# Optimization experiments

Hardware: AMD Instinct MI355X
Metric: run time of the kernel (lower is better)

The kernel has to match this reference:

```python
import jax, jax.numpy as jnp
import numpy as np

B = 4            # scenes
N = 100000       # points per scene
BN = B * N
M = 200000       # occupied target voxels
C_IMG = 64       # img_feat_dim
C_3D = 32        # INIT_DIM (3D feature width at p1 scale)
COORD_MAX = 256  # voxel grid extent per axis


def setup_inputs() -> dict:
    key = jax.random.key(0)
    k1, k2, k3, k4, k5, k6 = jax.random.split(key, 6)
    # batched voxel coords: col0 = batch idx, cols1:4 = xyz voxel coords
    bcol = jax.random.randint(k1, (M, 1), 0, B, dtype=jnp.int32)
    xyz = jax.random.randint(k2, (M, 3), 0, COORD_MAX, dtype=jnp.int32)
    tgt_coords = jnp.concatenate([bcol, xyz], axis=1)  # (M,4)
    # each point maps onto some target voxel (torch code asserts full validity)
    pts_idx = jax.random.randint(k3, (BN,), 0, M, dtype=jnp.int32)
    pfeat = jax.random.normal(k4, (BN, C_IMG), dtype=jnp.float32)
    tgt_feats = jax.random.normal(k5, (M, C_3D), dtype=jnp.float32)
    W_fuse = jax.random.normal(k6, (C_3D + C_IMG, C_3D), dtype=jnp.float32) * 0.05
    b_fuse = jnp.zeros((C_3D,), dtype=jnp.float32)
    return {"pfeat": pfeat, "tgt_feats": tgt_feats, "W_fuse": W_fuse,
            "b_fuse": b_fuse, "tgt_coords": tgt_coords, "pts_idx": pts_idx}


def reference(pfeat, tgt_feats, W_fuse, b_fuse, tgt_coords, pts_idx):
    # point voxel coords (stride-snapped in torch; identity here since points map to voxels)
    pts_coords = tgt_coords[pts_idx]                              # (BN,4)
    # --- key packing (mirrors _pack_keys with shift-to-nonnegative) ---
    xyz_all = jnp.concatenate([pts_coords[:, 1:], tgt_coords[:, 1:]], axis=0)
    shift = jnp.maximum(-xyz_all.min(axis=0), 0)
    pts_xyz = pts_coords[:, 1:] + shift
    tgt_xyz = tgt_coords[:, 1:] + shift
    max_xyz = jnp.maximum(pts_xyz.max(axis=0), tgt_xyz.max(axis=0))
    mx, my, mz = max_xyz[0] + 1, max_xyz[1] + 1, max_xyz[2] + 1

    def pack(b, xyz):
        return ((b * mx + xyz[:, 0]) * my + xyz[:, 1]) * mz + xyz[:, 2]

    pts_key = pack(pts_coords[:, 0], pts_xyz)                     # (BN,)
    tgt_key = pack(tgt_coords[:, 0], tgt_xyz)                     # (M,)
    # --- sort target keys, binary-search point keys (torch.sort + searchsorted) ---
    order = jnp.argsort(tgt_key)
    tgt_key_sorted = tgt_key[order]
    pos = jnp.minimum(jnp.searchsorted(tgt_key_sorted, pts_key), M - 1)
    tgt_idx = order[pos]                                          # (BN,) voxel each point lands in
    # --- scatter-mean of 2D point features into voxels (_scatter_mean) ---
    sums = jax.ops.segment_sum(pfeat, tgt_idx, num_segments=M)    # (M,C_IMG)
    cnt = jax.ops.segment_sum(jnp.ones((pfeat.shape[0], 1), pfeat.dtype),
                              tgt_idx, num_segments=M)            # (M,1)
    img_feat_u = sums / jnp.maximum(cnt, 1.0)
    # --- ME.cat + 1x1 MinkowskiConvolution fuse == concat + matmul ---
    fused = jnp.concatenate([tgt_feats, img_feat_u], axis=1)      # (M, C_3D+C_IMG)
    return fused @ W_fuse + b_fuse                                # (M, C_3D)
```

## Files before the change

kernel.cpp:

```cpp
#include <hip/hip_runtime.h>

#define HBITS 19
#define HSIZE (1u << HBITS)
#define HMASK (HSIZE - 1u)
#define EMPTY_KEY 0xFFFFFFFFu
#define SLOTS 8

__device__ __forceinline__ unsigned hash_key(unsigned k) {
    return (k * 2654435761u) >> (32 - HBITS);
}

__device__ __forceinline__ unsigned pack_key(int4 c) {
    return ((unsigned)c.x << 24) | ((unsigned)c.y << 16) |
           ((unsigned)c.z << 8) | (unsigned)c.w;
}

__global__ __launch_bounds__(256)
void build_hash(const int4* __restrict__ tgt_coords, int M,
                uint2* __restrict__ htab) {
    int v = blockIdx.x * blockDim.x + threadIdx.x;
    if (v >= M) return;
    unsigned key = pack_key(tgt_coords[v]);
    unsigned h = hash_key(key);
    while (true) {
        unsigned prev = atomicCAS(&htab[h].x, EMPTY_KEY, key);
        if (prev == EMPTY_KEY || prev == key) {
            atomicMin(&htab[h].y, (unsigned)v);
            break;
        }
        h = (h + 1u) & HMASK;
    }
}

__global__ __launch_bounds__(256)
void fill_slots(const int* __restrict__ pts_idx,
                const int4* __restrict__ tgt_coords,
                const uint2* __restrict__ htab,
                int BN,
                int* __restrict__ cnt,
                int* __restrict__ slotbuf,
                int* __restrict__ ohead,
                int* __restrict__ nxt) {
    int p = blockIdx.x * blockDim.x + threadIdx.x;
    if (p >= BN) return;
    int vox = pts_idx[p];
    unsigned key = pack_key(tgt_coords[vox]);
    unsigned h = hash_key(key);
    uint2 e = htab[h];
    while (e.x != key) { h = (h + 1u) & HMASK; e = htab[h]; }
    int c = (int)e.y;
    int idx = atomicAdd(&cnt[c], 1) + 1;
    if (idx < SLOTS) slotbuf[c * SLOTS + idx] = p;
    else             nxt[p] = atomicExch(&ohead[c], p);
}

#define VPB 8
__global__ __launch_bounds__(256)
void gather_mean(const float2* __restrict__ pf2,
                 const int* __restrict__ cnt,
                 const int4* __restrict__ slot4,
                 const int* __restrict__ ohead,
                 const int* __restrict__ nxt,
                 int M,
                 float2* __restrict__ mean2) {
    int t = threadIdx.x;
    int grp = t >> 5;
    int g   = t & 31;
    int v = blockIdx.x * VPB + grp;
    if (v >= M) return;

    int n = cnt[v] + 1;
    int4 sa = make_int4(0, 0, 0, 0), sb = make_int4(0, 0, 0, 0);
    if (n > 0) sa = slot4[(size_t)v * 2];
    if (n > 4) sb = slot4[(size_t)v * 2 + 1];
    float2 f0 = {0,0}, f1 = {0,0}, f2 = {0,0}, f3 = {0,0};
    float2 f4 = {0,0}, f5 = {0,0}, f6 = {0,0}, f7 = {0,0};
    if (n > 0) f0 = pf2[(size_t)sa.x * 32 + g];
    if (n > 1) f1 = pf2[(size_t)sa.y * 32 + g];
    if (n > 2) f2 = pf2[(size_t)sa.z * 32 + g];
    if (n > 3) f3 = pf2[(size_t)sa.w * 32 + g];
    if (n > 4) f4 = pf2[(size_t)sb.x * 32 + g];
    if (n > 5) f5 = pf2[(size_t)sb.y * 32 + g];
    if (n > 6) f6 = pf2[(size_t)sb.z * 32 + g];
    if (n > 7) f7 = pf2[(size_t)sb.w * 32 + g];
    float sx = ((f0.x + f1.x) + (f2.x + f3.x)) + ((f4.x + f5.x) + (f6.x + f7.x));
    float sy = ((f0.y + f1.y) + (f2.y + f3.y)) + ((f4.y + f5.y) + (f6.y + f7.y));
    if (n > SLOTS) {
        int p = ohead[v];
        while (p >= 0) {
            float2 f = pf2[(size_t)p * 32 + g];
            sx += f.x; sy += f.y;
            p = nxt[p];
        }
    }
    float inv = 1.0f / fmaxf((float)n, 1.0f);
    mean2[(size_t)v * 32 + g] = make_float2(sx * inv, sy * inv);
}

__global__ __launch_bounds__(256)
void matmul_scalar(const float4* __restrict__ tgt4,
                   const float4* __restrict__ mean4,
                   const float* __restrict__ W,
                   const float* __restrict__ bias,
                   int M,
                   float4* __restrict__ out4) {
    int v = blockIdx.x * blockDim.x + threadIdx.x;
    if (v >= M) return;

    float acc[32];
#pragma unroll
    for (int oc = 0; oc < 32; ++oc) acc[oc] = bias[oc];

    const float4* xr = tgt4 + (size_t)v * 8;
#pragma unroll 2
    for (int k4 = 0; k4 < 8; ++k4) {
        float4 x = xr[k4];
        const float* w0 = W + k4 * 4 * 32;
#pragma unroll
        for (int oc = 0; oc < 32; ++oc) {
            acc[oc] = fmaf(x.x, w0[oc],      acc[oc]);
            acc[oc] = fmaf(x.y, w0[32 + oc], acc[oc]);
            acc[oc] = fmaf(x.z, w0[64 + oc], acc[oc]);
            acc[oc] = fmaf(x.w, w0[96 + oc], acc[oc]);
        }
    }
    const float4* mr = mean4 + (size_t)v * 16;
#pragma unroll 2
    for (int k4 = 0; k4 < 16; ++k4) {
        float4 x = mr[k4];
        const float* w0 = W + (32 + k4 * 4) * 32;
#pragma unroll
        for (int oc = 0; oc < 32; ++oc) {
            acc[oc] = fmaf(x.x, w0[oc],      acc[oc]);
            acc[oc] = fmaf(x.y, w0[32 + oc], acc[oc]);
            acc[oc] = fmaf(x.z, w0[64 + oc], acc[oc]);
            acc[oc] = fmaf(x.w, w0[96 + oc], acc[oc]);
        }
    }

    float4* o = out4 + (size_t)v * 8;
#pragma unroll
    for (int q = 0; q < 8; ++q)
        o[q] = make_float4(acc[4 * q], acc[4 * q + 1], acc[4 * q + 2], acc[4 * q + 3]);
}

extern "C" void kernel_launch(void* const* d_in, const int* in_sizes, int n_in,
                              void* d_out, int out_size, void* d_ws, size_t ws_size,
                              hipStream_t stream) {
    const float* pfeat      = (const float*)d_in[0];
    const float* tgt_feats  = (const float*)d_in[1];
    const float* W_fuse     = (const float*)d_in[2];
    const float* b_fuse     = (const float*)d_in[3];
    const int*   tgt_coords = (const int*)d_in[4];
    const int*   pts_idx    = (const int*)d_in[5];
    float* out = (float*)d_out;

    const int M  = in_sizes[4] / 4;
    const int BN = in_sizes[5];

    char* ws = (char*)d_ws;
    uint2* htab    = (uint2*)ws;
    size_t off = (size_t)HSIZE * 8;
    int*   cnt     = (int*)(ws + off);              off += (size_t)M * 4;
    int*   ohead   = (int*)(ws + off);              off += (size_t)M * 4;
    int*   slotbuf = (int*)(ws + off);              off += (size_t)M * SLOTS * 4;
    int*   nxt     = (int*)(ws + off);              off += (size_t)BN * 4;
    float* mean    = (float*)(ws + off);

    size_t ff_bytes = (size_t)HSIZE * 8 + (size_t)M * 8;
    hipMemsetAsync(htab, 0xFF, ff_bytes, stream);

    const int TB = 256;
    build_hash<<<(M + TB - 1) / TB, TB, 0, stream>>>(
        (const int4*)tgt_coords, M, htab);
    fill_slots<<<(BN + TB - 1) / TB, TB, 0, stream>>>(
        pts_idx, (const int4*)tgt_coords, htab, BN, cnt, slotbuf, ohead, nxt);
    gather_mean<<<(M + VPB - 1) / VPB, TB, 0, stream>>>(
        (const float2*)pfeat, cnt, (const int4*)slotbuf, ohead, nxt, M,
        (float2*)mean);
    matmul_scalar<<<(M + TB - 1) / TB, TB, 0, stream>>>(
        (const float4*)tgt_feats, (const float4*)mean, W_fuse, b_fuse, M,
        (float4*)out);
}
```

Baseline: 282.6 us.

## Fuse scatter-mean gather with the 1x1 fuse matmul via shared memory

Merges the gather_mean and matmul_scalar kernels into one kernel. Each 32-lane group stages its voxel's 3D features and mean image features in shared memory, then each lane computes one output channel using a register-held column of W. This removes the round trip of the mean buffer through global memory and one kernel launch. In exchange every thread loads 96 weights per block and there is a block-wide barrier.

```diff
diff --git a/kernel.cpp b/kernel.cpp
--- a/kernel.cpp
+++ b/kernel.cpp
@@ -56,92 +56,73 @@
 
 #define VPB 8
 __global__ __launch_bounds__(256)
-void gather_mean(const float2* __restrict__ pf2,
+void gather_fuse(const float2* __restrict__ pf2,
+                 const float* __restrict__ tgtf,
                  const int* __restrict__ cnt,
                  const int4* __restrict__ slot4,
                  const int* __restrict__ ohead,
                  const int* __restrict__ nxt,
+                 const float* __restrict__ W,
+                 const float* __restrict__ bias,
                  int M,
-                 float2* __restrict__ mean2) {
+                 float* __restrict__ out) {
+    __shared__ __align__(16) float xs[VPB][104];
+
     int t = threadIdx.x;
     int grp = t >> 5;
     int g   = t & 31;
     int v = blockIdx.x * VPB + grp;
-    if (v >= M) return;
+    bool valid = (v < M);
 
-    int n = cnt[v] + 1;
-    int4 sa = make_int4(0, 0, 0, 0), sb = make_int4(0, 0, 0, 0);
-    if (n > 0) sa = slot4[(size_t)v * 2];
-    if (n > 4) sb = slot4[(size_t)v * 2 + 1];
-    float2 f0 = {0,0}, f1 = {0,0}, f2 = {0,0}, f3 = {0,0};
-    float2 f4 = {0,0}, f5 = {0,0}, f6 = {0,0}, f7 = {0,0};
-    if (n > 0) f0 = pf2[(size_t)sa.x * 32 + g];
-    if (n > 1) f1 = pf2[(size_t)sa.y * 32 + g];
-    if (n > 2) f2 = pf2[(size_t)sa.z * 32 + g];
-    if (n > 3) f3 = pf2[(size_t)sa.w * 32 + g];
-    if (n > 4) f4 = pf2[(size_t)sb.x * 32 + g];
-    if (n > 5) f5 = pf2[(size_t)sb.y * 32 + g];
-    if (n > 6) f6 = pf2[(size_t)sb.z * 32 + g];
-    if (n > 7) f7 = pf2[(size_t)sb.w * 32 + g];
-    float sx = ((f0.x + f1.x) + (f2.x + f3.x)) + ((f4.x + f5.x) + (f6.x + f7.x));
-    float sy = ((f0.y + f1.y) + (f2.y + f3.y)) + ((f4.y + f5.y) + (f6.y + f7.y));
-    if (n > SLOTS) {
-        int p = ohead[v];
-        while (p >= 0) {
-            float2 f = pf2[(size_t)p * 32 + g];
-            sx += f.x; sy += f.y;
-            p = nxt[p];
+    if (valid) {
+        int n = cnt[v] + 1;
+        int4 sa = make_int4(0, 0, 0, 0), sb = make_int4(0, 0, 0, 0);
+        if (n > 0) sa = slot4[(size_t)v * 2];
+        if (n > 4) sb = slot4[(size_t)v * 2 + 1];
+        float2 f0 = {0,0}, f1 = {0,0}, f2 = {0,0}, f3 = {0,0};
+        float2 f4 = {0,0}, f5 = {0,0}, f6 = {0,0}, f7 = {0,0};
+        if (n > 0) f0 = pf2[(size_t)sa.x * 32 + g];
+        if (n > 1) f1 = pf2[(size_t)sa.y * 32 + g];
+        if (n > 2) f2 = pf2[(size_t)sa.z * 32 + g];
+        if (n > 3) f3 = pf2[(size_t)sa.w * 32 + g];
+        if (n > 4) f4 = pf2[(size_t)sb.x * 32 + g];
+        if (n > 5) f5 = pf2[(size_t)sb.y * 32 + g];
+        if (n > 6) f6 = pf2[(size_t)sb.z * 32 + g];
+        if (n > 7) f7 = pf2[(size_t)sb.w * 32 + g];
+        float sx = ((f0.x + f1.x) + (f2.x + f3.x)) + ((f4.x + f5.x) + (f6.x + f7.x));
+        float sy = ((f0.y + f1.y) + (f2.y + f3.y)) + ((f4.y + f5.y) + (f6.y + f7.y));
+        if (n > SLOTS) {
+            int p = ohead[v];
+            while (p >= 0) {
+                float2 f = pf2[(size_t)p * 32 + g];
+                sx += f.x; sy += f.y;
+                p = nxt[p];
+            }
         }
-    }
-    float inv = 1.0f / fmaxf((float)n, 1.0f);
-    mean2[(size_t)v * 32 + g] = make_float2(sx * inv, sy * inv);
-}
-
-__global__ __launch_bounds__(256)
-void matmul_scalar(const float4* __restrict__ tgt4,
-                   const float4* __restrict__ mean4,
-                   const float* __restrict__ W,
-                   const float* __restrict__ bias,
-                   int M,
-                   float4* __restrict__ out4) {
-    int v = blockIdx.x * blockDim.x + threadIdx.x;
-    if (v >= M) return;
-
-    float acc[32];
-#pragma unroll
-    for (int oc = 0; oc < 32; ++oc) acc[oc] = bias[oc];
-
-    const float4* xr = tgt4 + (size_t)v * 8;
-#pragma unroll 2
-    for (int k4 = 0; k4 < 8; ++k4) {
-        float4 x = xr[k4];
-        const float* w0 = W + k4 * 4 * 32;
-#pragma unroll
-        for (int oc = 0; oc < 32; ++oc) {
-            acc[oc] = fmaf(x.x, w0[oc],      acc[oc]);
-            acc[oc] = fmaf(x.y, w0[32 + oc], acc[oc]);
-            acc[oc] = fmaf(x.z, w0[64 + oc], acc[oc]);
-            acc[oc] = fmaf(x.w, w0[96 + oc], acc[oc]);
-        }
-    }
-    const float4* mr = mean4 + (size_t)v * 16;
-#pragma unroll 2
-    for (int k4 = 0; k4 < 16; ++k4) {
-        float4 x = mr[k4];
-        const float* w0 = W + (32 + k4 * 4) * 32;
-#pragma unroll
-        for (int oc = 0; oc < 32; ++oc) {
-            acc[oc] = fmaf(x.x, w0[oc],      acc[oc]);
-            acc[oc] = fmaf(x.y, w0[32 + oc], acc[oc]);
-            acc[oc] = fmaf(x.z, w0[64 + oc], acc[oc]);
-            acc[oc] = fmaf(x.w, w0[96 + oc], acc[oc]);
-        }
+        float inv = 1.0f / fmaxf((float)n, 1.0f);
+        xs[grp][g] = tgtf[(size_t)v * 32 + g];
+        *reinterpret_cast<float2*>(&xs[grp][32 + 2 * g]) =
+            make_float2(sx * inv, sy * inv);
     }
 
-    float4* o = out4 + (size_t)v * 8;
+    float wcol[96];
 #pragma unroll
-    for (int q = 0; q < 8; ++q)
-        o[q] = make_float4(acc[4 * q], acc[4 * q + 1], acc[4 * q + 2], acc[4 * q + 3]);
+    for (int k = 0; k < 96; ++k) wcol[k] = W[k * 32 + g];
+
+    __syncthreads();
+
+    if (valid) {
+        float acc = bias[g];
+#pragma unroll
+        for (int k4 = 0; k4 < 24; ++k4) {
+            float4 x = *reinterpret_cast<const float4*>(&xs[grp][k4 * 4]);
+            acc = fmaf(x.x, wcol[4 * k4 + 0], acc);
+            acc = fmaf(x.y, wcol[4 * k4 + 1], acc);
+            acc = fmaf(x.z, wcol[4 * k4 + 2], acc);
+            acc = fmaf(x.w, wcol[4 * k4 + 3], acc);
+        }
+        out[(size_t)v * 32 + g] = acc;
+    }
 }
 
 extern "C" void kernel_launch(void* const* d_in, const int* in_sizes, int n_in,
@@ -164,8 +145,7 @@
     int*   cnt     = (int*)(ws + off);              off += (size_t)M * 4;
     int*   ohead   = (int*)(ws + off);              off += (size_t)M * 4;
     int*   slotbuf = (int*)(ws + off);              off += (size_t)M * SLOTS * 4;
-    int*   nxt     = (int*)(ws + off);              off += (size_t)BN * 4;
-    float* mean    = (float*)(ws + off);
+    int*   nxt     = (int*)(ws + off);
 
     size_t ff_bytes = (size_t)HSIZE * 8 + (size_t)M * 8;
     hipMemsetAsync(htab, 0xFF, ff_bytes, stream);
@@ -175,10 +155,7 @@
         (const int4*)tgt_coords, M, htab);
     fill_slots<<<(BN + TB - 1) / TB, TB, 0, stream>>>(
         pts_idx, (const int4*)tgt_coords, htab, BN, cnt, slotbuf, ohead, nxt);
-    gather_mean<<<(M + VPB - 1) / VPB, TB, 0, stream>>>(
-        (const float2*)pfeat, cnt, (const int4*)slotbuf, ohead, nxt, M,
-        (float2*)mean);
-    matmul_scalar<<<(M + TB - 1) / TB, TB, 0, stream>>>(
-        (const float4*)tgt_feats, (const float4*)mean, W_fuse, b_fuse, M,
-        (float4*)out);
+    gather_fuse<<<(M + VPB - 1) / VPB, TB, 0, stream>>>(
+        (const float2*)pfeat, tgt_feats, cnt, (const int4*)slotbuf, ohead, nxt,
+        W_fuse, b_fuse, M, out);
 }
```

Result: slower. 313.4 us (+10.9%).
